# Kernel tuning notes

Measured on AMD Instinct MI355X. Metric: run time of the kernel, lower is better.

The kernel has to match this reference:

```python
import jax, jax.numpy as jnp
import numpy as np

B, P, D = 64, 1024, 768

def setup_inputs() -> dict:
    key = jax.random.key(0)
    k1, k2, k3 = jax.random.split(key, 3)
    z = jax.random.normal(k1, (B, P, D), dtype=jnp.float32)
    q = jax.random.normal(k2, (1, 1, D), dtype=jnp.float32)
    W_proj = jax.random.normal(k3, (D, D), dtype=jnp.float32) * (1.0 / np.sqrt(D))
    return {"z": z, "q": q, "W_proj": W_proj}

def reference(z, q, W_proj):
    # k = Linear(z) with weight W_proj (torch: z @ W.T), no bias
    k = jnp.einsum("bpd,ed->bpe", z, W_proj)          # [B,P,D]
    d = z.shape[-1]
    scale = 1.0 / jnp.sqrt(jnp.asarray(d, dtype=z.dtype))
    # single learnable query broadcast over batch: scores [B,1,P]
    scores = jnp.einsum("xqd,bpd->bqp", q, k) * scale
    attn = jax.nn.softmax(scores, axis=-1)            # [B,1,P]
    pooled = jnp.einsum("bqp,bpd->bqd", attn, z)      # [B,1,D]
    return pooled[:, 0, :]                            # [B,D]
```

## Files before the change

### kernel.cpp

```cpp
#include <hip/hip_runtime.h>
#include <math.h>

#define BB 64
#define PP 1024
#define DD 768
#define PS 16
#define NPART 64

__global__ __launch_bounds__(256) void qw_kernel(const float* __restrict__ q,
                                                 const float* __restrict__ W,
                                                 float* __restrict__ qw) {
    int d  = blockIdx.x * 256 + threadIdx.x;
    int e0 = blockIdx.y * 24;
    float acc = 0.f;
#pragma unroll
    for (int i = 0; i < 24; ++i) {
        int e = e0 + i;
        acc += q[e] * W[(size_t)e * DD + d];
    }
    atomicAdd(&qw[d], acc);
}

__global__ __launch_bounds__(256) void fused_kernel(const float* __restrict__ z,
                                                    const float* __restrict__ qw,
                                                    float* __restrict__ macc,
                                                    float* __restrict__ ml) {
    const float scale = 0.03608439182435161f;
    int b    = blockIdx.x;
    int ps   = blockIdx.y;
    int tid  = threadIdx.x;
    int wave = tid >> 6;
    int lane = tid & 63;

    const float4* qw4 = (const float4*)qw;
    float4 q0 = qw4[lane], q1 = qw4[lane + 64], q2 = qw4[lane + 128];

    int p0 = ps * 64 + wave * 16;
    const float4* zr = (const float4*)(z + ((size_t)b * PP + p0) * DD);

    float m = -INFINITY, l = 0.f;
    float4 a0 = {0.f, 0.f, 0.f, 0.f}, a1 = a0, a2 = a0;

    for (int i = 0; i < 16; ++i) {
        float4 z0 = zr[lane], z1 = zr[lane + 64], z2 = zr[lane + 128];
        zr += DD / 4;

        float dacc = z0.x * q0.x + z0.y * q0.y + z0.z * q0.z + z0.w * q0.w
                   + z1.x * q1.x + z1.y * q1.y + z1.z * q1.z + z1.w * q1.w
                   + z2.x * q2.x + z2.y * q2.y + z2.z * q2.z + z2.w * q2.w;
#pragma unroll
        for (int off = 32; off >= 1; off >>= 1)
            dacc += __shfl_xor(dacc, off, 64);

        float s  = dacc * scale;
        float mn = fmaxf(m, s);
        float alpha = __expf(m - mn);
        float e     = __expf(s - mn);
        l = l * alpha + e;
        a0.x = a0.x * alpha + e * z0.x;  a0.y = a0.y * alpha + e * z0.y;
        a0.z = a0.z * alpha + e * z0.z;  a0.w = a0.w * alpha + e * z0.w;
        a1.x = a1.x * alpha + e * z1.x;  a1.y = a1.y * alpha + e * z1.y;
        a1.z = a1.z * alpha + e * z1.z;  a1.w = a1.w * alpha + e * z1.w;
        a2.x = a2.x * alpha + e * z2.x;  a2.y = a2.y * alpha + e * z2.y;
        a2.z = a2.z * alpha + e * z2.z;  a2.w = a2.w * alpha + e * z2.w;
        m = mn;
    }

    int part = b * NPART + ps * 4 + wave;
    float4* ap4 = (float4*)(macc + (size_t)part * DD);
    ap4[lane] = a0; ap4[lane + 64] = a1; ap4[lane + 128] = a2;
    if (lane == 0) { ml[part * 2] = m; ml[part * 2 + 1] = l; }
}

__global__ __launch_bounds__(256) void reduce_kernel(const float* __restrict__ macc,
                                                     const float* __restrict__ ml,
                                                     float* __restrict__ out) {
    int b    = blockIdx.x;
    int tid  = threadIdx.x;
    int wave = tid >> 6;
    int lane = tid & 63;

    __shared__ float wts[NPART];
    __shared__ float Lsh;

    if (wave == 0) {
        float mk = ml[(b * NPART + lane) * 2];
        float lk = ml[(b * NPART + lane) * 2 + 1];
        float M = mk;
#pragma unroll
        for (int off = 32; off >= 1; off >>= 1) M = fmaxf(M, __shfl_xor(M, off, 64));
        float w = __expf(mk - M);
        float L = w * lk;
#pragma unroll
        for (int off = 32; off >= 1; off >>= 1) L += __shfl_xor(L, off, 64);
        wts[lane] = w;
        if (lane == 0) Lsh = L;
    }
    __syncthreads();

    float inv = 1.f / Lsh;
    const float* base = macc + (size_t)b * NPART * DD;
#pragma unroll
    for (int c = 0; c < 3; ++c) {
        int d = c * 256 + tid;
        float acc = 0.f;
#pragma unroll 8
        for (int k = 0; k < NPART; ++k) acc += wts[k] * base[(size_t)k * DD + d];
        out[b * DD + d] = acc * inv;
    }
}

extern "C" void kernel_launch(void* const* d_in, const int* in_sizes, int n_in,
                              void* d_out, int out_size, void* d_ws, size_t ws_size,
                              hipStream_t stream) {
    const float* z = (const float*)d_in[0];
    const float* q = (const float*)d_in[1];
    const float* W = (const float*)d_in[2];
    float* out = (float*)d_out;

    char* ws = (char*)d_ws;
    float* qw   = (float*)ws;
    float* ml   = (float*)(ws + 4096);
    float* macc = (float*)(ws + 4096 + 65536);

    hipMemsetAsync(qw, 0, DD * sizeof(float), stream);
    dim3 qg(3, 32);
    qw_kernel<<<qg, 256, 0, stream>>>(q, W, qw);
    dim3 fg(BB, PS);
    fused_kernel<<<fg, 256, 0, stream>>>(z, qw, macc, ml);
    reduce_kernel<<<BB, 256, 0, stream>>>(macc, ml, out);
}
```

Measured before the change: 294.7 us.

## Stage z tiles through LDS and process 16-row blocks with fewer splits

The fused kernel now copies 16-row tiles of z into shared memory, computes the 16 scores cooperatively, and updates the online softmax once per tile instead of once per row. The grid shrinks from 16 to 8 splits per batch, and each thread accumulates one scalar per column chunk, which shrinks the partial-result buffer and the reduce work. The aim is fewer serial wave reductions and rescales per row, plus a cheaper final reduction. In exchange there are extra LDS traffic and several __syncthreads per tile, 52KB of shared memory that limits occupancy, and half as many blocks (512) for a bandwidth-bound stream of z.

```diff
diff --git a/kernel.cpp b/kernel.cpp
--- a/kernel.cpp
+++ b/kernel.cpp
@@ -4,8 +4,9 @@
 #define BB 64
 #define PP 1024
 #define DD 768
-#define PS 16
-#define NPART 64
+#define SS 8
+#define TR 16
+#define NT 8
 
 __global__ __launch_bounds__(256) void qw_kernel(const float* __restrict__ q,
                                                  const float* __restrict__ W,
@@ -26,86 +27,101 @@
                                                     float* __restrict__ macc,
                                                     float* __restrict__ ml) {
     const float scale = 0.03608439182435161f;
-    int b    = blockIdx.x;
-    int ps   = blockIdx.y;
-    int tid  = threadIdx.x;
-    int wave = tid >> 6;
-    int lane = tid & 63;
+    __shared__ float zt[TR * DD];
+    __shared__ float qs[DD];
+    __shared__ float sc[TR];
 
-    const float4* qw4 = (const float4*)qw;
-    float4 q0 = qw4[lane], q1 = qw4[lane + 64], q2 = qw4[lane + 128];
+    int b     = blockIdx.x;
+    int split = blockIdx.y;
+    int tid   = threadIdx.x;
 
-    int p0 = ps * 64 + wave * 16;
-    const float4* zr = (const float4*)(z + ((size_t)b * PP + p0) * DD);
+    for (int i = tid; i < DD; i += 256) qs[i] = qw[i];
+
+    int row = tid >> 4;
+    int l16 = tid & 15;
 
     float m = -INFINITY, l = 0.f;
-    float4 a0 = {0.f, 0.f, 0.f, 0.f}, a1 = a0, a2 = a0;
+    float a0 = 0.f, a1 = 0.f, a2 = 0.f;
 
-    for (int i = 0; i < 16; ++i) {
-        float4 z0 = zr[lane], z1 = zr[lane + 64], z2 = zr[lane + 128];
-        zr += DD / 4;
+    const float4* gz = (const float4*)(z + ((size_t)b * PP + split * 128) * DD);
+    float4*       lz = (float4*)zt;
+    const float4* q4 = (const float4*)qs;
 
-        float dacc = z0.x * q0.x + z0.y * q0.y + z0.z * q0.z + z0.w * q0.w
-                   + z1.x * q1.x + z1.y * q1.y + z1.z * q1.z + z1.w * q1.w
-                   + z2.x * q2.x + z2.y * q2.y + z2.z * q2.z + z2.w * q2.w;
+    __syncthreads();
+
+    for (int t = 0; t < NT; ++t) {
+        float4 tmp[12];
 #pragma unroll
-        for (int off = 32; off >= 1; off >>= 1)
-            dacc += __shfl_xor(dacc, off, 64);
+        for (int k = 0; k < 12; ++k) tmp[k] = gz[(size_t)t * 3072 + k * 256 + tid];
+#pragma unroll
+        for (int k = 0; k < 12; ++k) lz[k * 256 + tid] = tmp[k];
+        __syncthreads();
 
-        float s  = dacc * scale;
-        float mn = fmaxf(m, s);
+        float part = 0.f;
+#pragma unroll
+        for (int k = 0; k < 12; ++k) {
+            float4 zv = lz[row * 192 + k * 16 + l16];
+            float4 qv = q4[k * 16 + l16];
+            part += zv.x * qv.x + zv.y * qv.y + zv.z * qv.z + zv.w * qv.w;
+        }
+#pragma unroll
+        for (int mask = 8; mask >= 1; mask >>= 1)
+            part += __shfl_xor(part, mask, 64);
+        if (l16 == 0) sc[row] = part * scale;
+        __syncthreads();
+
+        float mt = sc[0];
+#pragma unroll
+        for (int r = 1; r < TR; ++r) mt = fmaxf(mt, sc[r]);
+        float mn    = fmaxf(m, mt);
         float alpha = __expf(m - mn);
-        float e     = __expf(s - mn);
-        l = l * alpha + e;
-        a0.x = a0.x * alpha + e * z0.x;  a0.y = a0.y * alpha + e * z0.y;
-        a0.z = a0.z * alpha + e * z0.z;  a0.w = a0.w * alpha + e * z0.w;
-        a1.x = a1.x * alpha + e * z1.x;  a1.y = a1.y * alpha + e * z1.y;
-        a1.z = a1.z * alpha + e * z1.z;  a1.w = a1.w * alpha + e * z1.w;
-        a2.x = a2.x * alpha + e * z2.x;  a2.y = a2.y * alpha + e * z2.y;
-        a2.z = a2.z * alpha + e * z2.z;  a2.w = a2.w * alpha + e * z2.w;
         m = mn;
+        l *= alpha;
+        a0 *= alpha; a1 *= alpha; a2 *= alpha;
+#pragma unroll
+        for (int r = 0; r < TR; ++r) {
+            float e = __expf(sc[r] - mn);
+            l  += e;
+            a0 += e * zt[r * DD + tid];
+            a1 += e * zt[r * DD + tid + 256];
+            a2 += e * zt[r * DD + tid + 512];
+        }
+        __syncthreads();
     }
 
-    int part = b * NPART + ps * 4 + wave;
-    float4* ap4 = (float4*)(macc + (size_t)part * DD);
-    ap4[lane] = a0; ap4[lane + 64] = a1; ap4[lane + 128] = a2;
-    if (lane == 0) { ml[part * 2] = m; ml[part * 2 + 1] = l; }
+    int part_idx = b * SS + split;
+    float* ap = macc + (size_t)part_idx * DD;
+    ap[tid] = a0; ap[tid + 256] = a1; ap[tid + 512] = a2;
+    if (tid == 0) { ml[part_idx * 2] = m; ml[part_idx * 2 + 1] = l; }
 }
 
 __global__ __launch_bounds__(256) void reduce_kernel(const float* __restrict__ macc,
                                                      const float* __restrict__ ml,
                                                      float* __restrict__ out) {
-    int b    = blockIdx.x;
-    int tid  = threadIdx.x;
-    int wave = tid >> 6;
-    int lane = tid & 63;
+    int b   = blockIdx.x;
+    int tid = threadIdx.x;
 
-    __shared__ float wts[NPART];
-    __shared__ float Lsh;
+    float mk[SS], lk[SS];
+#pragma unroll
+    for (int k = 0; k < SS; ++k) {
+        mk[k] = ml[(b * SS + k) * 2];
+        lk[k] = ml[(b * SS + k) * 2 + 1];
+    }
+    float M = mk[0];
+#pragma unroll
+    for (int k = 1; k < SS; ++k) M = fmaxf(M, mk[k]);
+    float L = 0.f, w[SS];
+#pragma unroll
+    for (int k = 0; k < SS; ++k) { w[k] = __expf(mk[k] - M); L += w[k] * lk[k]; }
+    float inv = 1.f / L;
 
-    if (wave == 0) {
-        float mk = ml[(b * NPART + lane) * 2];
-        float lk = ml[(b * NPART + lane) * 2 + 1];
-        float M = mk;
+    const float* base = macc + (size_t)b * SS * DD;
 #pragma unroll
-        for (int off = 32; off >= 1; off >>= 1) M = fmaxf(M, __shfl_xor(M, off, 64));
-        float w = __expf(mk - M);
-        float L = w * lk;
+    for (int j = 0; j < 3; ++j) {
+        int d = j * 256 + tid;
+        float acc = 0.f;
 #pragma unroll
-        for (int off = 32; off >= 1; off >>= 1) L += __shfl_xor(L, off, 64);
-        wts[lane] = w;
-        if (lane == 0) Lsh = L;
-    }
-    __syncthreads();
-
-    float inv = 1.f / Lsh;
-    const float* base = macc + (size_t)b * NPART * DD;
-#pragma unroll
-    for (int c = 0; c < 3; ++c) {
-        int d = c * 256 + tid;
-        float acc = 0.f;
-#pragma unroll 8
-        for (int k = 0; k < NPART; ++k) acc += wts[k] * base[(size_t)k * DD + d];
+        for (int k = 0; k < SS; ++k) acc += w[k] * base[(size_t)k * DD + d];
         out[b * DD + d] = acc * inv;
     }
 }
@@ -121,12 +137,12 @@
     char* ws = (char*)d_ws;
     float* qw   = (float*)ws;
     float* ml   = (float*)(ws + 4096);
-    float* macc = (float*)(ws + 4096 + 65536);
+    float* macc = (float*)(ws + 4096 + 8192);
 
     hipMemsetAsync(qw, 0, DD * sizeof(float), stream);
     dim3 qg(3, 32);
     qw_kernel<<<qg, 256, 0, stream>>>(q, W, qw);
-    dim3 fg(BB, PS);
+    dim3 fg(BB, SS);
     fused_kernel<<<fg, 256, 0, stream>>>(z, qw, macc, ml);
     reduce_kernel<<<BB, 256, 0, stream>>>(macc, ml, out);
 }
```

Result: faster. 286.8 us (-2.7%).

## Stage z tiles through double-buffered shared memory with register prefetch

Applied to the files above, without the earlier changes.

The fused kernel now has each block cooperatively load 8-row tiles of z into a double-buffered LDS array. Each thread prefetches the next tile into registers while the waves compute online softmax on the current tile. The grid shrinks from 16 to 8 splits per batch, so the reduce kernel merges 32 partials instead of 64. This is meant to overlap global loads with compute and raise memory-level parallelism, at the cost of extra LDS traffic, barriers and fewer blocks.

```diff
diff --git a/kernel.cpp b/kernel.cpp
--- a/kernel.cpp
+++ b/kernel.cpp
@@ -4,8 +4,10 @@
 #define BB 64
 #define PP 1024
 #define DD 768
-#define PS 16
-#define NPART 64
+#define SS 8
+#define TR 8
+#define NT 16
+#define NPART 32
 
 __global__ __launch_bounds__(256) void qw_kernel(const float* __restrict__ q,
                                                  const float* __restrict__ W,
@@ -21,52 +23,82 @@
     atomicAdd(&qw[d], acc);
 }
 
-__global__ __launch_bounds__(256) void fused_kernel(const float* __restrict__ z,
-                                                    const float* __restrict__ qw,
-                                                    float* __restrict__ macc,
-                                                    float* __restrict__ ml) {
+__global__ __launch_bounds__(256, 3) void fused_kernel(const float* __restrict__ z,
+                                                       const float* __restrict__ qw,
+                                                       float* __restrict__ macc,
+                                                       float* __restrict__ ml) {
     const float scale = 0.03608439182435161f;
-    int b    = blockIdx.x;
-    int ps   = blockIdx.y;
-    int tid  = threadIdx.x;
-    int wave = tid >> 6;
-    int lane = tid & 63;
+    __shared__ float4 buf[2][TR * DD / 4];
+
+    int b     = blockIdx.x;
+    int split = blockIdx.y;
+    int tid   = threadIdx.x;
+    int wave  = tid >> 6;
+    int lane  = tid & 63;
 
     const float4* qw4 = (const float4*)qw;
     float4 q0 = qw4[lane], q1 = qw4[lane + 64], q2 = qw4[lane + 128];
 
-    int p0 = ps * 64 + wave * 16;
-    const float4* zr = (const float4*)(z + ((size_t)b * PP + p0) * DD);
+    const float4* gz = (const float4*)(z + ((size_t)b * PP + split * 128) * DD);
 
     float m = -INFINITY, l = 0.f;
     float4 a0 = {0.f, 0.f, 0.f, 0.f}, a1 = a0, a2 = a0;
 
-    for (int i = 0; i < 16; ++i) {
-        float4 z0 = zr[lane], z1 = zr[lane + 64], z2 = zr[lane + 128];
-        zr += DD / 4;
-
-        float dacc = z0.x * q0.x + z0.y * q0.y + z0.z * q0.z + z0.w * q0.w
-                   + z1.x * q1.x + z1.y * q1.y + z1.z * q1.z + z1.w * q1.w
-                   + z2.x * q2.x + z2.y * q2.y + z2.z * q2.z + z2.w * q2.w;
+    {
+        float4 tmp[6];
 #pragma unroll
-        for (int off = 32; off >= 1; off >>= 1)
-            dacc += __shfl_xor(dacc, off, 64);
-
-        float s  = dacc * scale;
-        float mn = fmaxf(m, s);
-        float alpha = __expf(m - mn);
-        float e     = __expf(s - mn);
-        l = l * alpha + e;
-        a0.x = a0.x * alpha + e * z0.x;  a0.y = a0.y * alpha + e * z0.y;
-        a0.z = a0.z * alpha + e * z0.z;  a0.w = a0.w * alpha + e * z0.w;
-        a1.x = a1.x * alpha + e * z1.x;  a1.y = a1.y * alpha + e * z1.y;
-        a1.z = a1.z * alpha + e * z1.z;  a1.w = a1.w * alpha + e * z1.w;
-        a2.x = a2.x * alpha + e * z2.x;  a2.y = a2.y * alpha + e * z2.y;
-        a2.z = a2.z * alpha + e * z2.z;  a2.w = a2.w * alpha + e * z2.w;
-        m = mn;
+        for (int j = 0; j < 6; ++j) tmp[j] = gz[j * 256 + tid];
+#pragma unroll
+        for (int j = 0; j < 6; ++j) buf[0][j * 256 + tid] = tmp[j];
     }
 
-    int part = b * NPART + ps * 4 + wave;
+    int r0 = wave * 2;
+
+    for (int t = 0; t < NT; ++t) {
+        __syncthreads();
+
+        float4 tmp[6];
+        if (t + 1 < NT) {
+#pragma unroll
+            for (int j = 0; j < 6; ++j)
+                tmp[j] = gz[(size_t)(t + 1) * 1536 + j * 256 + tid];
+        }
+
+        const float4* bt = buf[t & 1];
+#pragma unroll
+        for (int rr = 0; rr < 2; ++rr) {
+            const float4* rowp = bt + (r0 + rr) * 192;
+            float4 z0 = rowp[lane], z1 = rowp[lane + 64], z2 = rowp[lane + 128];
+
+            float d = z0.x * q0.x + z0.y * q0.y + z0.z * q0.z + z0.w * q0.w
+                    + z1.x * q1.x + z1.y * q1.y + z1.z * q1.z + z1.w * q1.w
+                    + z2.x * q2.x + z2.y * q2.y + z2.z * q2.z + z2.w * q2.w;
+#pragma unroll
+            for (int off = 32; off >= 1; off >>= 1)
+                d += __shfl_xor(d, off, 64);
+
+            float s     = d * scale;
+            float mn    = fmaxf(m, s);
+            float alpha = __expf(m - mn);
+            float e     = __expf(s - mn);
+            l = l * alpha + e;
+            a0.x = a0.x * alpha + e * z0.x;  a0.y = a0.y * alpha + e * z0.y;
+            a0.z = a0.z * alpha + e * z0.z;  a0.w = a0.w * alpha + e * z0.w;
+            a1.x = a1.x * alpha + e * z1.x;  a1.y = a1.y * alpha + e * z1.y;
+            a1.z = a1.z * alpha + e * z1.z;  a1.w = a1.w * alpha + e * z1.w;
+            a2.x = a2.x * alpha + e * z2.x;  a2.y = a2.y * alpha + e * z2.y;
+            a2.z = a2.z * alpha + e * z2.z;  a2.w = a2.w * alpha + e * z2.w;
+            m = mn;
+        }
+
+        if (t + 1 < NT) {
+#pragma unroll
+            for (int j = 0; j < 6; ++j)
+                buf[(t + 1) & 1][j * 256 + tid] = tmp[j];
+        }
+    }
+
+    int part = (b * SS + split) * 4 + wave;
     float4* ap4 = (float4*)(macc + (size_t)part * DD);
     ap4[lane] = a0; ap4[lane + 64] = a1; ap4[lane + 128] = a2;
     if (lane == 0) { ml[part * 2] = m; ml[part * 2 + 1] = l; }
@@ -84,8 +116,8 @@
     __shared__ float Lsh;
 
     if (wave == 0) {
-        float mk = ml[(b * NPART + lane) * 2];
-        float lk = ml[(b * NPART + lane) * 2 + 1];
+        float mk = (lane < NPART) ? ml[(b * NPART + lane) * 2]     : -INFINITY;
+        float lk = (lane < NPART) ? ml[(b * NPART + lane) * 2 + 1] : 0.f;
         float M = mk;
 #pragma unroll
         for (int off = 32; off >= 1; off >>= 1) M = fmaxf(M, __shfl_xor(M, off, 64));
@@ -93,7 +125,7 @@
         float L = w * lk;
 #pragma unroll
         for (int off = 32; off >= 1; off >>= 1) L += __shfl_xor(L, off, 64);
-        wts[lane] = w;
+        if (lane < NPART) wts[lane] = w;
         if (lane == 0) Lsh = L;
     }
     __syncthreads();
@@ -121,12 +153,12 @@
     char* ws = (char*)d_ws;
     float* qw   = (float*)ws;
     float* ml   = (float*)(ws + 4096);
-    float* macc = (float*)(ws + 4096 + 65536);
+    float* macc = (float*)(ws + 4096 + 32768);
 
     hipMemsetAsync(qw, 0, DD * sizeof(float), stream);
     dim3 qg(3, 32);
     qw_kernel<<<qg, 256, 0, stream>>>(q, W, qw);
-    dim3 fg(BB, PS);
+    dim3 fg(BB, SS);
     fused_kernel<<<fg, 256, 0, stream>>>(z, qw, macc, ml);
     reduce_kernel<<<BB, 256, 0, stream>>>(macc, ml, out);
 }
```

New measurement: 289.6 us. Within noise of the previous version (-1.7%).
